# Optimization experiments

Hardware: AMD Instinct MI355X
Metric: run time of the kernel (lower is better)

Reference implementation:

```python
import jax, jax.numpy as jnp
import numpy as np

B, S, D, H = 4, 2048, 1024, 16
DK = D // H


def setup_inputs() -> dict:
    key = jax.random.key(0)
    ks = jax.random.split(key, 12)
    def lin(k):
        # torch nn.Linear default init scale ~ 1/sqrt(fan_in); use small normal
        return jax.random.normal(k, (D, D), dtype=jnp.float32) * (1.0 / np.sqrt(D))
    inp = {
        "query": jax.random.normal(ks[0], (B, S, D), dtype=jnp.float32),
        "key":   jax.random.normal(ks[1], (B, S, D), dtype=jnp.float32),
        "value": jax.random.normal(ks[2], (B, S, D), dtype=jnp.float32),
        "Wq": lin(ks[3]), "bq": jax.random.normal(ks[4], (D,), dtype=jnp.float32) * 0.01,
        "Wk": lin(ks[5]), "bk": jax.random.normal(ks[6], (D,), dtype=jnp.float32) * 0.01,
        "Wv": lin(ks[7]), "bv": jax.random.normal(ks[8], (D,), dtype=jnp.float32) * 0.01,
        "Wo": lin(ks[9]), "bo": jax.random.normal(ks[10], (D,), dtype=jnp.float32) * 0.01,
        # causal mask, True = attend (masked_fill where mask == 0)
        "causal_mask": jnp.tril(jnp.ones((S, S), dtype=bool))[None, None, :, :],
    }
    return inp


def reference(query, key, value, Wq, bq, Wk, bk, Wv, bv, Wo, bo, causal_mask):
    # Linear projections (torch Linear: y = x @ W.T + b), split heads -> [B,H,S,DK]
    def proj(x, W, b):
        return (x @ W.T + b).reshape(B, S, H, DK).transpose(0, 2, 1, 3)
    Q = proj(query, Wq, bq)
    K = proj(key, Wk, bk)
    V = proj(value, Wv, bv)
    scale = 1.0 / jnp.sqrt(jnp.float32(DK))
    scores = jnp.einsum('bhqd,bhkd->bhqk', Q, K) * scale  # [B,H,S,S]
    scores = jnp.where(causal_mask, scores, -jnp.inf)
    attn = jax.nn.softmax(scores, axis=-1)
    out = jnp.einsum('bhqk,bhkd->bhqd', attn, V)  # [B,H,S,DK]
    out = out.transpose(0, 2, 1, 3).reshape(B, S, D)
    return out @ Wo.T + bo
```

## Files before the change

### kernel.cpp

```cpp
#include <hip/hip_runtime.h>
#include <stdint.h>

#define SLEN   2048
#define DMODEL 1024
#define NHEAD  16
#define DKH    64
#define BATCH  4

typedef unsigned short ushort_t;
typedef __bf16         bf16x8 __attribute__((ext_vector_type(8)));
typedef unsigned short u16x8  __attribute__((ext_vector_type(8)));
typedef unsigned short u16x4  __attribute__((ext_vector_type(4)));
typedef unsigned int   u32x4  __attribute__((ext_vector_type(4)));
typedef float          f32x4  __attribute__((ext_vector_type(4)));

#define QSCALE 0.18033688f

__device__ __forceinline__ ushort_t f2bf(float f) {
  unsigned int u = __builtin_bit_cast(unsigned int, f);
  u += 0x7fffu + ((u >> 16) & 1u);
  return (ushort_t)(u >> 16);
}
__device__ __forceinline__ unsigned pk2(float a, float b) {
  const unsigned ua = __builtin_bit_cast(unsigned, a) + 0x8000u;
  const unsigned ub = __builtin_bit_cast(unsigned, b) + 0x8000u;
  return __builtin_amdgcn_perm(ub, ua, 0x07060302u);
}
__device__ __forceinline__ u16x8 cvt8f(const float* p) {
  f32x4 a = *(const f32x4*)p;
  f32x4 b = *(const f32x4*)(p + 4);
  u32x4 w;
  w[0] = pk2(a[0], a[1]);
  w[1] = pk2(a[2], a[3]);
  w[2] = pk2(b[0], b[1]);
  w[3] = pk2(b[2], b[3]);
  return __builtin_bit_cast(u16x8, w);
}

typedef __attribute__((address_space(1))) void gvoid_t;
typedef __attribute__((address_space(3))) void lvoid_t;
__device__ __forceinline__ void gld_lds16(const void* g, void* l) {
  __builtin_amdgcn_global_load_lds((gvoid_t*)(g), (lvoid_t*)(l), 16, 0, 0);
}

__device__ __forceinline__ int swz(int row, int c) {
  return row * 64 + (c ^ ((row & 7) * 8));
}
__device__ __forceinline__ int sx4(int r) { return (r ^ (r >> 2)) & 3; }

__global__ __launch_bounds__(256) void cvt_all(
    const float* __restrict__ Wq, const float* __restrict__ Wk,
    const float* __restrict__ Wv, const float* __restrict__ Wo,
    const float* __restrict__ q, const float* __restrict__ k,
    const float* __restrict__ v,
    ushort_t* __restrict__ Wbf, ushort_t* __restrict__ Xq,
    ushort_t* __restrict__ Xk,  ushort_t* __restrict__ Xv) {
  const int b = blockIdx.x;
  if (b < 2048) {
    const int gid = b * 256 + threadIdx.x;
    const int seg = gid >> 17;
    const int off = (gid & 131071) * 8;
    const float* src = (seg == 0) ? Wq : (seg == 1) ? Wk : (seg == 2) ? Wv : Wo;
    *(u16x8*)&Wbf[((size_t)seg << 20) + off] = cvt8f(src + off);
  } else {
    const int gid = (b - 2048) * 256 + threadIdx.x;
    const int seg = gid >> 20;
    const size_t off = (size_t)(gid & 1048575) * 8;
    const float* src = (seg == 0) ? q : (seg == 1) ? k : v;
    ushort_t*    dst = (seg == 0) ? Xq : (seg == 1) ? Xk : Xv;
    *(u16x8*)&dst[off] = cvt8f(src + off);
  }
}

__device__ __forceinline__ void gemm_body(
    const ushort_t* __restrict__ X, const ushort_t* __restrict__ W,
    const float* __restrict__ bias, void* __restrict__ Outv, const int mode,
    const float sc)
{
  __shared__ ushort_t lA[3][128 * 32];
  __shared__ ushort_t lB[3][256 * 32];

  const int t    = threadIdx.x;
  const int lane = t & 63;
  const int w    = t >> 6;
  const int wm   = (w >> 1) * 64;
  const int wn   = (w & 1) * 128;
  const int m0   = blockIdx.x * 128;
  const int n0   = blockIdx.y * 256;
  const int col  = lane & 15;
  const int quad = lane >> 4;

  f32x4 acc[4][8];
#pragma unroll
  for (int i = 0; i < 4; i++)
#pragma unroll
    for (int j = 0; j < 8; j++) acc[i][j] = f32x4{0.f, 0.f, 0.f, 0.f};

  const int rA   = t >> 2;
  const int csrc = ((t & 3) ^ sx4(rA)) * 8;
  const ushort_t* gA0 = X + (size_t)(m0 + rA) * DMODEL + csrc;
  const ushort_t* gA1 = gA0 + (size_t)64 * DMODEL;
  const ushort_t* gB0 = W + (size_t)(n0 + rA) * DMODEL + csrc;
  const ushort_t* gB1 = gB0 + (size_t)64 * DMODEL;
  const ushort_t* gB2 = gB0 + (size_t)128 * DMODEL;
  const ushort_t* gB3 = gB0 + (size_t)192 * DMODEL;

#define STAGE_G(buf, k0) do {                        \
    gld_lds16(gB0 + (k0), &lB[buf][t * 8]);          \
    gld_lds16(gB1 + (k0), &lB[buf][t * 8 + 2048]);   \
    gld_lds16(gB2 + (k0), &lB[buf][t * 8 + 4096]);   \
    gld_lds16(gB3 + (k0), &lB[buf][t * 8 + 6144]);   \
    gld_lds16(gA0 + (k0), &lA[buf][t * 8]);          \
    gld_lds16(gA1 + (k0), &lA[buf][t * 8 + 2048]);   \
  } while (0)

  const int rchunk = (quad ^ ((col ^ (col >> 2)) & 3)) * 8;

  STAGE_G(0, 0);
  STAGE_G(1, 32);

  const int NT = DMODEL / 32;
  int cur = 0;
  for (int ks = 0; ks < NT; ++ks) {
    if (ks + 1 < NT) {
      asm volatile("s_waitcnt vmcnt(6)" ::: "memory");
    } else {
      asm volatile("s_waitcnt vmcnt(0)" ::: "memory");
    }
    __builtin_amdgcn_s_barrier();
    __builtin_amdgcn_sched_barrier(0);

    if (ks + 2 < NT) {
      const int nb = (cur == 0) ? 2 : cur - 1;
      STAGE_G(nb, (ks + 2) * 32);
    }

    const ushort_t* cA = &lA[cur][0];
    const ushort_t* cB = &lB[cur][0];
    bf16x8 af[4], bfr[8];
#pragma unroll
    for (int mi = 0; mi < 4; mi++)
      af[mi] = __builtin_bit_cast(bf16x8,
          *(const u16x8*)&cA[(wm + mi * 16 + col) * 32 + rchunk]);
#pragma unroll
    for (int ni = 0; ni < 8; ni++)
      bfr[ni] = __builtin_bit_cast(bf16x8,
          *(const u16x8*)&cB[(wn + ni * 16 + col) * 32 + rchunk]);

#pragma unroll
    for (int mi = 0; mi < 4; mi++)
#pragma unroll
      for (int ni = 0; ni < 8; ni++)
        acc[mi][ni] = __builtin_amdgcn_mfma_f32_16x16x32_bf16(
            af[mi], bfr[ni], acc[mi][ni], 0, 0, 0);

    cur = (cur == 2) ? 0 : cur + 1;
  }
#undef STAGE_G

  const int b_ = (m0 + wm) >> 11;
#pragma unroll
  for (int ni = 0; ni < 8; ni++) {
    const int n  = n0 + wn + ni * 16 + col;
    const float bn = bias[n];
    const float bns = bn * sc;
    const int h  = n >> 6, dk = n & (DKH - 1);
#pragma unroll
    for (int mi = 0; mi < 4; mi++) {
      if (mode == 2) {
        const int s0 = ((m0 + wm + mi * 16 + quad * 4) & (SLEN - 1));
        u16x4 pk;
#pragma unroll
        for (int r = 0; r < 4; r++) pk[r] = f2bf(acc[mi][ni][r] + bn);
        *(u16x4*)&((ushort_t*)Outv)[(((size_t)(b_ * NHEAD + h)) * DKH + dk) * SLEN + s0] = pk;
      } else if (mode == 1) {
#pragma unroll
        for (int r = 0; r < 4; r++) {
          const int m = m0 + wm + mi * 16 + quad * 4 + r;
          const int s = m & (SLEN - 1);
          ((ushort_t*)Outv)[(((size_t)(b_ * NHEAD + h)) * SLEN + s) * DKH + dk] =
              f2bf(fmaf(acc[mi][ni][r], sc, bns));
        }
      } else {
#pragma unroll
        for (int r = 0; r < 4; r++) {
          const int m = m0 + wm + mi * 16 + quad * 4 + r;
          ((float*)Outv)[(size_t)m * DMODEL + n] = acc[mi][ni][r] + bn;
        }
      }
    }
  }
}

__global__ __launch_bounds__(256) void gemm_qkv(
    const ushort_t* Xq, const ushort_t* Xk, const ushort_t* Xv,
    const ushort_t* Wbf,
    const float* bq, const float* bk, const float* bv,
    ushort_t* Qh, ushort_t* Kh, ushort_t* VhT) {
  const int z = blockIdx.z;
  const ushort_t* X = (z == 0) ? Xq : (z == 1) ? Xk : Xv;
  const ushort_t* W = Wbf + ((size_t)z << 20);
  const float* bias = (z == 0) ? bq : (z == 1) ? bk : bv;
  ushort_t* out     = (z == 0) ? Qh : (z == 1) ? Kh : VhT;
  gemm_body(X, W, bias, out, (z == 2) ? 2 : 1, (z == 0) ? QSCALE : 1.0f);
}

__global__ __launch_bounds__(256) void gemm_out(
    const ushort_t* X, const ushort_t* Wobf, const float* bo, float* Out) {
  gemm_body(X, Wobf, bo, Out, 0, 1.0f);
}

__global__ __launch_bounds__(256, 4) void flash_attn(
    const ushort_t* __restrict__ Qh, const ushort_t* __restrict__ Kh,
    const ushort_t* __restrict__ VhT, ushort_t* __restrict__ Out)
{
  __shared__ ushort_t lK[2 * 64 * 64];
  __shared__ ushort_t lV[2 * 64 * 64];
  __shared__ ushort_t lP[4 * 16 * 64];

  const int t    = threadIdx.x;
  const int lane = t & 63;
  const int w    = t >> 6;
  const int col  = lane & 15;
  const int quad = lane >> 4;
  const int bh   = blockIdx.y;
  const int x    = blockIdx.x;
  const int ntA  = x + 1;
  const int ntB  = 32 - x;
  const int q0A  = x * 64;
  const int q0B  = (31 - x) * 64;

  const ushort_t* Qb = Qh  + (size_t)bh * SLEN * DKH;
  const ushort_t* Kb = Kh  + (size_t)bh * SLEN * DKH;
  const ushort_t* Vt = VhT + (size_t)bh * DKH * SLEN;

  bf16x8 qfA[2], qfB[2];
  {
    const int ra = q0A + w * 16 + col;
    const int rb = q0B + w * 16 + col;
    qfA[0] = __builtin_bit_cast(bf16x8, *(const u16x8*)&Qb[(size_t)ra * DKH + quad * 8]);
    qfA[1] = __builtin_bit_cast(bf16x8, *(const u16x8*)&Qb[(size_t)ra * DKH + 32 + quad * 8]);
    qfB[0] = __builtin_bit_cast(bf16x8, *(const u16x8*)&Qb[(size_t)rb * DKH + quad * 8]);
    qfB[1] = __builtin_bit_cast(bf16x8, *(const u16x8*)&Qb[(size_t)rb * DKH + 32 + quad * 8]);
  }

  f32x4 accA[4], accB[4], laccA, laccB;
#pragma unroll
  for (int n2 = 0; n2 < 4; n2++) {
    accA[n2] = f32x4{0.f, 0.f, 0.f, 0.f};
    accB[n2] = f32x4{0.f, 0.f, 0.f, 0.f};
  }
  laccA = f32x4{0.f, 0.f, 0.f, 0.f};
  laccB = f32x4{0.f, 0.f, 0.f, 0.f};

  u16x8 ones_u;
#pragma unroll
  for (int i = 0; i < 8; ++i) ones_u[i] = 0x3F80;
  const bf16x8 onesf = __builtin_bit_cast(bf16x8, ones_u);

  const int fA   = t * 8;
  const int rowA = fA >> 6;
  const int innA = fA & 63;
  const int cA   = innA ^ ((rowA & 7) * 8);
  const int rowB = rowA + 32;
  const int cB   = innA ^ ((rowB & 7) * 8);
  const ushort_t* gK0 = Kb + (size_t)rowA * DKH + cA;
  const ushort_t* gK1 = Kb + (size_t)rowB * DKH + cB;
  const ushort_t* gV0 = Vt + (size_t)rowA * SLEN + cA;
  const ushort_t* gV1 = Vt + (size_t)rowB * SLEN + cB;
  ushort_t* sK0 = &lK[fA];
  ushort_t* sK1 = &lK[fA + 2048];
  ushort_t* sV0 = &lV[fA];
  ushort_t* sV1 = &lV[fA + 2048];

  ushort_t* lPw = &lP[w * 1024];

  auto compute = [&](const bf16x8* qf, f32x4* acc_o, f32x4& lacc,
                     const int q0, const bool diag, const int kb,
                     const ushort_t* Kc, const ushort_t* Vc) {
    f32x4 sacc[4];
#pragma unroll
    for (int nt = 0; nt < 4; nt++) sacc[nt] = f32x4{0.f, 0.f, 0.f, 0.f};
#pragma unroll
    for (int ks = 0; ks < 2; ++ks) {
#pragma unroll
      for (int nt = 0; nt < 4; ++nt) {
        bf16x8 kf = __builtin_bit_cast(bf16x8,
            *(const u16x8*)&Kc[swz(nt * 16 + col, ks * 32 + quad * 8)]);
        sacc[nt] = __builtin_amdgcn_mfma_f32_16x16x32_bf16(qf[ks], kf, sacc[nt], 0, 0, 0);
      }
    }
#pragma unroll
    for (int r = 0; r < 4; r++) {
#pragma unroll
      for (int nt = 0; nt < 4; nt++) {
        float p = exp2f(sacc[nt][r]);
        if (diag) {
          const int kg = kb + nt * 16 + col;
          const int qg = q0 + w * 16 + quad * 4 + r;
          if (kg > qg) p = 0.f;
        }
        lPw[swz(quad * 4 + r, nt * 16 + col)] = f2bf(p);
      }
    }
    asm volatile("s_waitcnt lgkmcnt(0)" ::: "memory");
#pragma unroll
    for (int ks = 0; ks < 2; ++ks) {
      bf16x8 pf = __builtin_bit_cast(bf16x8,
          *(const u16x8*)&lPw[swz(col, ks * 32 + quad * 8)]);
      lacc = __builtin_amdgcn_mfma_f32_16x16x32_bf16(pf, onesf, lacc, 0, 0, 0);
#pragma unroll
      for (int n2 = 0; n2 < 4; ++n2) {
        bf16x8 vf = __builtin_bit_cast(bf16x8,
            *(const u16x8*)&Vc[swz(n2 * 16 + col, ks * 32 + quad * 8)]);
        acc_o[n2] = __builtin_amdgcn_mfma_f32_16x16x32_bf16(pf, vf, acc_o[n2], 0, 0, 0);
      }
    }
  };

  gld_lds16(gK0, sK0);
  gld_lds16(gK1, sK1);
  gld_lds16(gV0, sV0);
  gld_lds16(gV1, sV1);

  for (int it = 0; it < ntB; ++it) {
    const int cur = it & 1;
    const int kb  = it * 64;
    const ushort_t* Kc = &lK[cur * 4096];
    const ushort_t* Vc = &lV[cur * 4096];

    if (it + 1 < ntB) {
      const size_t kb1 = (size_t)(it + 1) * 64;
      const int nb = (cur ^ 1) * 4096;
      gld_lds16(gK0 + kb1 * DKH, sK0 + nb);
      gld_lds16(gK1 + kb1 * DKH, sK1 + nb);
      gld_lds16(gV0 + kb1,       sV0 + nb);
      gld_lds16(gV1 + kb1,       sV1 + nb);
      asm volatile("s_waitcnt vmcnt(4)" ::: "memory");
    } else {
      asm volatile("s_waitcnt vmcnt(0)" ::: "memory");
    }
    __builtin_amdgcn_s_barrier();

    compute(qfB, accB, laccB, q0B, it == ntB - 1, kb, Kc, Vc);
    if (it < ntA)
      compute(qfA, accA, laccA, q0A, it == ntA - 1, kb, Kc, Vc);

    __builtin_amdgcn_s_barrier();
  }

  const int b_ = bh >> 4;
  const int h  = bh & (NHEAD - 1);
#pragma unroll
  for (int side = 0; side < 2; ++side) {
    const f32x4* ao = side ? accA : accB;
    const f32x4& la = side ? laccA : laccB;
    const int q0 = side ? q0A : q0B;
#pragma unroll
    for (int r = 0; r < 4; r++) {
      const int qg = q0 + w * 16 + quad * 4 + r;
      const float inv = 1.f / la[r];
#pragma unroll
      for (int n2 = 0; n2 < 4; n2++) {
        const size_t oidx = ((size_t)b_ * SLEN + qg) * DMODEL + h * DKH + n2 * 16 + col;
        Out[oidx] = f2bf(ao[n2][r] * inv);
      }
    }
  }
}

extern "C" void kernel_launch(void* const* d_in, const int* in_sizes, int n_in,
                              void* d_out, int out_size, void* d_ws, size_t ws_size,
                              hipStream_t stream) {
  (void)in_sizes; (void)n_in; (void)out_size; (void)ws_size;
  const float* q  = (const float*)d_in[0];
  const float* k  = (const float*)d_in[1];
  const float* v  = (const float*)d_in[2];
  const float* Wq = (const float*)d_in[3];
  const float* bq = (const float*)d_in[4];
  const float* Wk = (const float*)d_in[5];
  const float* bk = (const float*)d_in[6];
  const float* Wv = (const float*)d_in[7];
  const float* bv = (const float*)d_in[8];
  const float* Wo = (const float*)d_in[9];
  const float* bo = (const float*)d_in[10];

  ushort_t* ws = (ushort_t*)d_ws;
  const size_t NELEM = (size_t)BATCH * SLEN * DMODEL;
  ushort_t* Wbf = ws;
  ushort_t* Qh  = ws + 4 * (1u << 20);
  ushort_t* Kh  = Qh + NELEM;
  ushort_t* Xq  = Kh + NELEM;
  ushort_t* Xk  = Xq + NELEM;
  ushort_t* Ao  = Xq;
  ushort_t* VhT = (ushort_t*)d_out;
  ushort_t* Xv  = (ushort_t*)d_out + NELEM;

  hipLaunchKernelGGL(cvt_all, dim3(2048 + 12288), dim3(256), 0, stream,
                     Wq, Wk, Wv, Wo, q, k, v, Wbf, Xq, Xk, Xv);
  hipLaunchKernelGGL(gemm_qkv, dim3(64, 4, 3), dim3(256), 0, stream,
                     Xq, Xk, Xv, Wbf, bq, bk, bv, Qh, Kh, VhT);
  hipLaunchKernelGGL(flash_attn, dim3(16, BATCH * NHEAD), dim3(256), 0, stream,
                     Qh, Kh, VhT, Ao);
  hipLaunchKernelGGL(gemm_out, dim3(64, 4), dim3(256), 0, stream,
                     Ao, Wbf + (3u << 20), bo, (float*)d_out);
}
```

Baseline: 386.6 us.

## Enlarge GEMM tiles to 256x256 with 8 waves and MFMA priority boost

The projection GEMMs now use 256x256 block tiles with 512 threads (8 waves arranged 2x4, each computing 128x64) instead of 128x256 tiles with 4 waves. Each thread issues 4 global-to-LDS loads per stage instead of 6, the vmcnt wait is adjusted to match, and s_setprio raises wave priority around the MFMA loop. The goal is more operand reuse per byte loaded and fewer global loads per FLOP. In exchange LDS use grows to about 96KB per block and the grid halves, so the QKV GEMM gets 384 blocks and the output GEMM only 128, which risks underfilling the CUs.

```diff
diff --git a/kernel.cpp b/kernel.cpp
--- a/kernel.cpp
+++ b/kernel.cpp
@@ -77,41 +77,37 @@
     const float* __restrict__ bias, void* __restrict__ Outv, const int mode,
     const float sc)
 {
-  __shared__ ushort_t lA[3][128 * 32];
+  __shared__ ushort_t lA[3][256 * 32];
   __shared__ ushort_t lB[3][256 * 32];
 
   const int t    = threadIdx.x;
   const int lane = t & 63;
   const int w    = t >> 6;
-  const int wm   = (w >> 1) * 64;
-  const int wn   = (w & 1) * 128;
-  const int m0   = blockIdx.x * 128;
+  const int wr   = w >> 2;
+  const int wc   = w & 3;
+  const int m0   = blockIdx.x * 256;
   const int n0   = blockIdx.y * 256;
   const int col  = lane & 15;
   const int quad = lane >> 4;
 
-  f32x4 acc[4][8];
-#pragma unroll
-  for (int i = 0; i < 4; i++)
-#pragma unroll
-    for (int j = 0; j < 8; j++) acc[i][j] = f32x4{0.f, 0.f, 0.f, 0.f};
-
-  const int rA   = t >> 2;
-  const int csrc = ((t & 3) ^ sx4(rA)) * 8;
-  const ushort_t* gA0 = X + (size_t)(m0 + rA) * DMODEL + csrc;
-  const ushort_t* gA1 = gA0 + (size_t)64 * DMODEL;
-  const ushort_t* gB0 = W + (size_t)(n0 + rA) * DMODEL + csrc;
-  const ushort_t* gB1 = gB0 + (size_t)64 * DMODEL;
-  const ushort_t* gB2 = gB0 + (size_t)128 * DMODEL;
-  const ushort_t* gB3 = gB0 + (size_t)192 * DMODEL;
+  f32x4 acc[8][4];
+#pragma unroll
+  for (int i = 0; i < 8; i++)
+#pragma unroll
+    for (int j = 0; j < 4; j++) acc[i][j] = f32x4{0.f, 0.f, 0.f, 0.f};
+
+  const int rS   = t >> 2;
+  const int cS   = ((t & 3) ^ sx4(rS)) * 8;
+  const ushort_t* gA0 = X + (size_t)(m0 + rS) * DMODEL + cS;
+  const ushort_t* gA1 = gA0 + (size_t)128 * DMODEL;
+  const ushort_t* gB0 = W + (size_t)(n0 + rS) * DMODEL + cS;
+  const ushort_t* gB1 = gB0 + (size_t)128 * DMODEL;
 
 #define STAGE_G(buf, k0) do {                        \
+    gld_lds16(gA0 + (k0), &lA[buf][t * 8]);          \
+    gld_lds16(gA1 + (k0), &lA[buf][t * 8 + 4096]);   \
     gld_lds16(gB0 + (k0), &lB[buf][t * 8]);          \
-    gld_lds16(gB1 + (k0), &lB[buf][t * 8 + 2048]);   \
-    gld_lds16(gB2 + (k0), &lB[buf][t * 8 + 4096]);   \
-    gld_lds16(gB3 + (k0), &lB[buf][t * 8 + 6144]);   \
-    gld_lds16(gA0 + (k0), &lA[buf][t * 8]);          \
-    gld_lds16(gA1 + (k0), &lA[buf][t * 8 + 2048]);   \
+    gld_lds16(gB1 + (k0), &lB[buf][t * 8 + 4096]);   \
   } while (0)
 
   const int rchunk = (quad ^ ((col ^ (col >> 2)) & 3)) * 8;
@@ -123,7 +119,7 @@
   int cur = 0;
   for (int ks = 0; ks < NT; ++ks) {
     if (ks + 1 < NT) {
-      asm volatile("s_waitcnt vmcnt(6)" ::: "memory");
+      asm volatile("s_waitcnt vmcnt(4)" ::: "memory");
     } else {
       asm volatile("s_waitcnt vmcnt(0)" ::: "memory");
     }
@@ -137,38 +133,40 @@
 
     const ushort_t* cA = &lA[cur][0];
     const ushort_t* cB = &lB[cur][0];
-    bf16x8 af[4], bfr[8];
-#pragma unroll
-    for (int mi = 0; mi < 4; mi++)
+    bf16x8 af[8], bfr[4];
+#pragma unroll
+    for (int mi = 0; mi < 8; mi++)
       af[mi] = __builtin_bit_cast(bf16x8,
-          *(const u16x8*)&cA[(wm + mi * 16 + col) * 32 + rchunk]);
-#pragma unroll
-    for (int ni = 0; ni < 8; ni++)
+          *(const u16x8*)&cA[(wr * 128 + mi * 16 + col) * 32 + rchunk]);
+#pragma unroll
+    for (int ni = 0; ni < 4; ni++)
       bfr[ni] = __builtin_bit_cast(bf16x8,
-          *(const u16x8*)&cB[(wn + ni * 16 + col) * 32 + rchunk]);
-
-#pragma unroll
-    for (int mi = 0; mi < 4; mi++)
-#pragma unroll
-      for (int ni = 0; ni < 8; ni++)
+          *(const u16x8*)&cB[(wc * 64 + ni * 16 + col) * 32 + rchunk]);
+
+    __builtin_amdgcn_s_setprio(1);
+#pragma unroll
+    for (int mi = 0; mi < 8; mi++)
+#pragma unroll
+      for (int ni = 0; ni < 4; ni++)
         acc[mi][ni] = __builtin_amdgcn_mfma_f32_16x16x32_bf16(
             af[mi], bfr[ni], acc[mi][ni], 0, 0, 0);
+    __builtin_amdgcn_s_setprio(0);
 
     cur = (cur == 2) ? 0 : cur + 1;
   }
 #undef STAGE_G
 
-  const int b_ = (m0 + wm) >> 11;
-#pragma unroll
-  for (int ni = 0; ni < 8; ni++) {
-    const int n  = n0 + wn + ni * 16 + col;
+  const int b_ = (m0 + wr * 128) >> 11;
+#pragma unroll
+  for (int ni = 0; ni < 4; ni++) {
+    const int n  = n0 + wc * 64 + ni * 16 + col;
     const float bn = bias[n];
     const float bns = bn * sc;
     const int h  = n >> 6, dk = n & (DKH - 1);
 #pragma unroll
-    for (int mi = 0; mi < 4; mi++) {
+    for (int mi = 0; mi < 8; mi++) {
       if (mode == 2) {
-        const int s0 = ((m0 + wm + mi * 16 + quad * 4) & (SLEN - 1));
+        const int s0 = ((m0 + wr * 128 + mi * 16 + quad * 4) & (SLEN - 1));
         u16x4 pk;
 #pragma unroll
         for (int r = 0; r < 4; r++) pk[r] = f2bf(acc[mi][ni][r] + bn);
@@ -176,7 +174,7 @@
       } else if (mode == 1) {
 #pragma unroll
         for (int r = 0; r < 4; r++) {
-          const int m = m0 + wm + mi * 16 + quad * 4 + r;
+          const int m = m0 + wr * 128 + mi * 16 + quad * 4 + r;
           const int s = m & (SLEN - 1);
           ((ushort_t*)Outv)[(((size_t)(b_ * NHEAD + h)) * SLEN + s) * DKH + dk] =
               f2bf(fmaf(acc[mi][ni][r], sc, bns));
@@ -184,7 +182,7 @@
       } else {
 #pragma unroll
         for (int r = 0; r < 4; r++) {
-          const int m = m0 + wm + mi * 16 + quad * 4 + r;
+          const int m = m0 + wr * 128 + mi * 16 + quad * 4 + r;
           ((float*)Outv)[(size_t)m * DMODEL + n] = acc[mi][ni][r] + bn;
         }
       }
@@ -192,7 +190,7 @@
   }
 }
 
-__global__ __launch_bounds__(256) void gemm_qkv(
+__global__ __launch_bounds__(512, 2) void gemm_qkv(
     const ushort_t* Xq, const ushort_t* Xk, const ushort_t* Xv,
     const ushort_t* Wbf,
     const float* bq, const float* bk, const float* bv,
@@ -205,7 +203,7 @@
   gemm_body(X, W, bias, out, (z == 2) ? 2 : 1, (z == 0) ? QSCALE : 1.0f);
 }
 
-__global__ __launch_bounds__(256) void gemm_out(
+__global__ __launch_bounds__(512, 2) void gemm_out(
     const ushort_t* X, const ushort_t* Wobf, const float* bo, float* Out) {
   gemm_body(X, Wobf, bo, Out, 0, 1.0f);
 }
@@ -398,10 +396,10 @@
 
   hipLaunchKernelGGL(cvt_all, dim3(2048 + 12288), dim3(256), 0, stream,
                      Wq, Wk, Wv, Wo, q, k, v, Wbf, Xq, Xk, Xv);
-  hipLaunchKernelGGL(gemm_qkv, dim3(64, 4, 3), dim3(256), 0, stream,
+  hipLaunchKernelGGL(gemm_qkv, dim3(32, 4, 3), dim3(512), 0, stream,
                      Xq, Xk, Xv, Wbf, bq, bk, bv, Qh, Kh, VhT);
   hipLaunchKernelGGL(flash_attn, dim3(16, BATCH * NHEAD), dim3(256), 0, stream,
                      Qh, Kh, VhT, Ao);
-  hipLaunchKernelGGL(gemm_out, dim3(64, 4), dim3(256), 0, stream,
+  hipLaunchKernelGGL(gemm_out, dim3(32, 4), dim3(512), 0, stream,
                      Ao, Wbf + (3u << 20), bo, (float*)d_out);
 }
```

Result: slower. 395.5 us (+2.3%).
